# Kernel tuning notes

Hardware: AMD Instinct MI355X
Metric: run time of the kernel (lower is better)

## Reference

```python
import jax, jax.numpy as jnp
import numpy as np

LN_EPS = 1e-5
NEG_SLOPE = 0.01

def layer_norm(h, gamma, beta):
    mu = jnp.mean(h, axis=-1, keepdims=True)
    var = jnp.var(h, axis=-1, keepdims=True)
    return (h - mu) * jax.lax.rsqrt(var + LN_EPS) * gamma + beta

def setup_inputs() -> dict:
    key = jax.random.key(0)
    ks = jax.random.split(key, 12)
    N, E = 50000, 600000
    D_NODE, D_EDGE, D_IN = 128, 64, 192  # D_IN = D_NODE + D_EDGE
    x = jax.random.normal(ks[0], (N, D_NODE), dtype=jnp.float32)
    edge_index = jax.random.randint(ks[1], (2, E), 0, N, dtype=jnp.int64)
    edge_attr = jax.random.normal(ks[2], (E, D_EDGE), dtype=jnp.float32)
    # mlp_before_agg: Linear(192->128) + LayerNorm + LeakyReLU
    W1 = jax.random.normal(ks[3], (D_IN, D_NODE), dtype=jnp.float32) / np.sqrt(D_IN)
    b1 = jnp.zeros((D_NODE,), dtype=jnp.float32)
    g1 = jnp.ones((D_NODE,), dtype=jnp.float32)
    be1 = jnp.zeros((D_NODE,), dtype=jnp.float32)
    # mlp_after_agg: Linear(128->128) + LayerNorm + LeakyReLU
    W2 = jax.random.normal(ks[4], (D_NODE, D_NODE), dtype=jnp.float32) / np.sqrt(D_NODE)
    b2 = jnp.zeros((D_NODE,), dtype=jnp.float32)
    g2 = jnp.ones((D_NODE,), dtype=jnp.float32)
    be2 = jnp.zeros((D_NODE,), dtype=jnp.float32)
    return {"x": x, "edge_index": edge_index, "edge_attr": edge_attr,
            "W1": W1, "b1": b1, "g1": g1, "be1": be1,
            "W2": W2, "b2": b2, "g2": g2, "be2": be2}

def reference(x, edge_index, edge_attr, W1, b1, g1, be1, W2, b2, g2, be2):
    N = x.shape[0]
    row, col = edge_index[0], edge_index[1]
    # 1. gather + concat: (E, D_NODE + D_EDGE)
    out = jnp.concatenate([x[row], edge_attr], axis=1)
    # 2. pre-agg MLP: Linear + LayerNorm + LeakyReLU
    out = jax.nn.leaky_relu(layer_norm(out @ W1 + b1, g1, be1), NEG_SLOPE)
    # 3. scatter-mean aggregate over destination nodes (empty segments -> 0)
    sums = jax.ops.segment_sum(out, col, num_segments=N)
    counts = jax.ops.segment_sum(jnp.ones((out.shape[0], 1), out.dtype), col, num_segments=N)
    out = sums / jnp.maximum(counts, 1.0)
    # 4. post-agg MLP + residual + activation
    out = jax.nn.leaky_relu(layer_norm(out @ W2 + b2, g2, be2), NEG_SLOPE)
    return jax.nn.leaky_relu(out + x, NEG_SLOPE)
```

## Files before the change

kernel.cpp:

```cpp
#include <hip/hip_runtime.h>

#define D_NODE 128
#define D_EDGE 64
#define D_IN   192
#define NEG    0.01f
#define LN_EPS 1e-5f

typedef short bf16x8 __attribute__((ext_vector_type(8)));
typedef float f32x4  __attribute__((ext_vector_type(4)));

__device__ __forceinline__ unsigned f2bf(float f) {
    unsigned u = __builtin_bit_cast(unsigned, f);
    return (u + 0x7FFFu + ((u >> 16) & 1u)) >> 16;
}
__device__ __forceinline__ unsigned pk2(float a, float b) {
    return f2bf(a) | (f2bf(b) << 16);
}
__device__ __forceinline__ float bf2f(unsigned short s) {
    unsigned u = ((unsigned)s) << 16;
    return __builtin_bit_cast(float, u);
}

__global__ void k_hist(const int* __restrict__ ei, int* __restrict__ hist, int E) {
    int i = blockIdx.x * blockDim.x + threadIdx.x;
    int stride = gridDim.x * blockDim.x;
    for (int e = i; e < E; e += stride) atomicAdd(&hist[ei[E + e]], 1);
}

__global__ __launch_bounds__(1024) void k_scanA(const int* __restrict__ hist,
                                                int* __restrict__ base,
                                                int* __restrict__ blockTot, int N) {
    __shared__ int wsum[16], woff[16];
    const int t = threadIdx.x, b = blockIdx.x;
    const int i = b * 1024 + t;
    const int lane = t & 63, w = t >> 6;
    int v = (i < N) ? hist[i] : 0;
    int x = v;
    #pragma unroll
    for (int d = 1; d < 64; d <<= 1) { int u = __shfl_up(x, d); if (lane >= d) x += u; }
    if (lane == 63) wsum[w] = x;
    __syncthreads();
    if (t < 16) {
        int y = wsum[t];
        #pragma unroll
        for (int d = 1; d < 16; d <<= 1) { int u = __shfl_up(y, d, 16); if (t >= d) y += u; }
        woff[t] = y - wsum[t];
    }
    __syncthreads();
    int incl = x + woff[w];
    if (i < N) base[i] = incl - v;
    if (t == 1023) blockTot[b] = incl;
}

__global__ void k_scanB(int* __restrict__ blockTot, int NB) {
    int t = threadIdx.x;
    int v = (t < NB) ? blockTot[t] : 0;
    int x = v;
    #pragma unroll
    for (int d = 1; d < 64; d <<= 1) { int u = __shfl_up(x, d); if (t >= d) x += u; }
    if (t < NB) blockTot[t] = x - v;
}

__global__ __launch_bounds__(1024) void k_scanC(int* __restrict__ base,
                                                const int* __restrict__ blockTot, int N) {
    int i = blockIdx.x * 1024 + threadIdx.x;
    if (i < N) base[i] += blockTot[blockIdx.x];
}

__global__ void k_bucket(const int* __restrict__ ei, int* __restrict__ base,
                         int* __restrict__ perm, int* __restrict__ srcrow,
                         int* __restrict__ dstcol, int E) {
    int i = blockIdx.x * blockDim.x + threadIdx.x;
    int stride = gridDim.x * blockDim.x;
    for (int e = i; e < E; e += stride) {
        int c = ei[E + e];
        int r = ei[e];
        int p = atomicAdd(&base[c], 1);
        perm[p]   = e;
        srcrow[p] = r;
        dstcol[p] = c;
    }
}

__global__ __launch_bounds__(256) void edge_mfma_seg(
    const float* __restrict__ x,
    const float* __restrict__ edge_attr,
    const int*   __restrict__ perm,
    const int*   __restrict__ srcrow,
    const int*   __restrict__ dstcol,
    const float* __restrict__ W1,
    const float* __restrict__ b1,
    const float* __restrict__ g1,
    const float* __restrict__ be1,
    float* __restrict__ sums,
    int E, int ntiles)
{
    __shared__ unsigned short h[64][200];
    __shared__ float rS [64][4], rS2[64][4];
    __shared__ int   scol[64];
    __shared__ unsigned long long maskSh;

    const int tid = threadIdx.x;
    const int w   = tid >> 6;
    const int l   = tid & 63;
    const int lm  = l & 15;
    const int q   = l >> 4;
    const int q8  = q * 8;

    bf16x8 Bfr[2][6];
    float  b1v[2], g1v[2], bev[2];
    #pragma unroll
    for (int c2 = 0; c2 < 2; ++c2) {
        const int n = (2 * w + c2) * 16 + lm;
        b1v[c2] = b1[n]; g1v[c2] = g1[n]; bev[c2] = be1[n];
        #pragma unroll
        for (int kt = 0; kt < 6; ++kt) {
            bf16x8 f;
            #pragma unroll
            for (int j = 0; j < 8; ++j)
                f[j] = (short)f2bf(W1[(kt * 32 + q8 + j) * 128 + n]);
            Bfr[c2][kt] = f;
        }
    }

    for (int tile = blockIdx.x; tile < ntiles; tile += gridDim.x) {
        const int e0 = tile * 64;

        {
            const int e  = tid >> 2;
            const int qq = tid & 3;
            const int ge = e0 + e;
            if (ge < E) {
                const int row = srcrow[ge];
                const int eid = perm[ge];
                const float4* xr = (const float4*)(x + (size_t)row * D_NODE);
                #pragma unroll
                for (int i = 0; i < 8; ++i) {
                    float4 v = xr[qq * 8 + i];
                    *(uint2*)&h[e][qq * 32 + i * 4] =
                        make_uint2(pk2(v.x, v.y), pk2(v.z, v.w));
                }
                const float4* ar = (const float4*)(edge_attr + (size_t)eid * D_EDGE);
                #pragma unroll
                for (int i = 0; i < 4; ++i) {
                    float4 v = ar[qq * 4 + i];
                    *(uint2*)&h[e][128 + qq * 16 + i * 4] =
                        make_uint2(pk2(v.x, v.y), pk2(v.z, v.w));
                }
            } else {
                #pragma unroll
                for (int i = 0; i < 8; ++i)
                    *(uint2*)&h[e][qq * 32 + i * 4] = make_uint2(0u, 0u);
                #pragma unroll
                for (int i = 0; i < 4; ++i)
                    *(uint2*)&h[e][128 + qq * 16 + i * 4] = make_uint2(0u, 0u);
            }
            if (tid < 64)
                scol[tid] = (e0 + tid < E) ? dstcol[e0 + tid] : -1;
        }
        __syncthreads();

        f32x4 acc[4][2];
        #pragma unroll
        for (int et = 0; et < 4; ++et)
            #pragma unroll
            for (int c2 = 0; c2 < 2; ++c2)
                acc[et][c2] = (f32x4){0.f, 0.f, 0.f, 0.f};

        #pragma unroll
        for (int et = 0; et < 4; ++et) {
            bf16x8 Afr[6];
            #pragma unroll
            for (int kt = 0; kt < 6; ++kt)
                Afr[kt] = *(const bf16x8*)&h[et * 16 + lm][kt * 32 + q8];
            #pragma unroll
            for (int c2 = 0; c2 < 2; ++c2)
                #pragma unroll
                for (int kt = 0; kt < 6; ++kt)
                    acc[et][c2] = __builtin_amdgcn_mfma_f32_16x16x32_bf16(
                        Afr[kt], Bfr[c2][kt], acc[et][c2], 0, 0, 0);
        }

        #pragma unroll
        for (int et = 0; et < 4; ++et) {
            #pragma unroll
            for (int r = 0; r < 4; ++r) {
                float v0 = acc[et][0][r] + b1v[0];
                float v1 = acc[et][1][r] + b1v[1];
                acc[et][0][r] = v0;
                acc[et][1][r] = v1;
                float s  = v0 + v1;
                float s2 = v0 * v0 + v1 * v1;
                #pragma unroll
                for (int off = 1; off < 16; off <<= 1) {
                    s  += __shfl_xor(s,  off, 16);
                    s2 += __shfl_xor(s2, off, 16);
                }
                if (lm == 0) {
                    const int em = et * 16 + q * 4 + r;
                    rS [em][w] = s;
                    rS2[em][w] = s2;
                }
            }
        }
        __syncthreads();

        if (tid < 64) {
            int me = scol[tid];
            int pv = (tid == 0) ? (me ^ 1) : scol[tid - 1];
            unsigned long long m = __ballot(me != pv);
            if (tid == 0) maskSh = m;
        }

        #pragma unroll
        for (int et = 0; et < 4; ++et) {
            #pragma unroll
            for (int r = 0; r < 4; ++r) {
                const int em = et * 16 + q * 4 + r;
                float4 p  = *(const float4*)&rS [em][0];
                float4 p2 = *(const float4*)&rS2[em][0];
                const float S    = (p.x  + p.y)  + (p.z  + p.w);
                const float S2   = (p2.x + p2.y) + (p2.z + p2.w);
                const float mu   = S * (1.f / 128.f);
                const float var  = S2 * (1.f / 128.f) - mu * mu;
                const float rstd = rsqrtf(var + LN_EPS);
                #pragma unroll
                for (int c2 = 0; c2 < 2; ++c2) {
                    float y = (acc[et][c2][r] - mu) * rstd * g1v[c2] + bev[c2];
                    y = (y > 0.f) ? y : NEG * y;
                    h[em][(2 * w + c2) * 16 + lm] = (unsigned short)f2bf(y);
                }
            }
        }
        __syncthreads();

        {
            const unsigned long long mask = maskSh;
            const int g  = tid >> 7;
            const int j  = tid & 127;
            const int lo = g * 32, hi = lo + 32;
            float s = 0.f;
            int rs = lo;
            for (int em = lo; em < hi; ++em) {
                s += bf2f(h[em][j]);
                const int nx = em + 1;
                const bool isEnd = (nx == hi) || ((mask >> nx) & 1ull);
                if (isEnd) {
                    const int dest = scol[em];
                    if (dest >= 0) {
                        const bool sg = (rs > 0) && ((mask >> rs) & 1ull);
                        const bool eg = (em < 63) && ((mask >> nx) & 1ull);
                        float* p = &sums[(size_t)dest * D_NODE + j];
                        if (sg && eg) *p = s;
                        else          atomicAdd(p, s);
                    }
                    s = 0.f; rs = nx;
                }
            }
        }
        __syncthreads();
    }
}

__global__ __launch_bounds__(256) void node_mfma(
    const float* __restrict__ sums,
    const int*   __restrict__ hist,
    const float* __restrict__ x,
    const float* __restrict__ W2,
    const float* __restrict__ b2,
    const float* __restrict__ g2,
    const float* __restrict__ be2,
    float* __restrict__ out,
    int N)
{
    __shared__ unsigned short h[64][136];
    __shared__ float rS [64][4], rS2[64][4];

    const int tid = threadIdx.x;
    const int w   = tid >> 6;
    const int l   = tid & 63;
    const int lm  = l & 15;
    const int q   = l >> 4;
    const int q8  = q * 8;

    bf16x8 Bfr[2][4];
    float  b2v[2], g2v[2], bev[2];
    #pragma unroll
    for (int c2 = 0; c2 < 2; ++c2) {
        const int n = (2 * w + c2) * 16 + lm;
        b2v[c2] = b2[n]; g2v[c2] = g2[n]; bev[c2] = be2[n];
        #pragma unroll
        for (int kt = 0; kt < 4; ++kt) {
            bf16x8 f;
            #pragma unroll
            for (int j = 0; j < 8; ++j)
                f[j] = (short)f2bf(W2[(kt * 32 + q8 + j) * 128 + n]);
            Bfr[c2][kt] = f;
        }
    }

    const int n0 = blockIdx.x * 64;

    {
        const int e  = tid >> 2;
        const int qq = tid & 3;
        const int gn = n0 + e;
        if (gn < N) {
            const int cnt = hist[gn];
            const float sc = (cnt > 0) ? 1.f / (float)cnt : 0.f;
            const float4* sr = (const float4*)(sums + (size_t)gn * D_NODE);
            #pragma unroll
            for (int i = 0; i < 8; ++i) {
                float4 v = sr[qq * 8 + i];
                *(uint2*)&h[e][qq * 32 + i * 4] =
                    make_uint2(pk2(v.x * sc, v.y * sc), pk2(v.z * sc, v.w * sc));
            }
        } else {
            #pragma unroll
            for (int i = 0; i < 8; ++i)
                *(uint2*)&h[e][qq * 32 + i * 4] = make_uint2(0u, 0u);
        }
    }
    __syncthreads();

    f32x4 acc[4][2];
    #pragma unroll
    for (int et = 0; et < 4; ++et)
        #pragma unroll
        for (int c2 = 0; c2 < 2; ++c2)
            acc[et][c2] = (f32x4){0.f, 0.f, 0.f, 0.f};

    #pragma unroll
    for (int et = 0; et < 4; ++et) {
        bf16x8 Afr[4];
        #pragma unroll
        for (int kt = 0; kt < 4; ++kt)
            Afr[kt] = *(const bf16x8*)&h[et * 16 + lm][kt * 32 + q8];
        #pragma unroll
        for (int c2 = 0; c2 < 2; ++c2)
            #pragma unroll
            for (int kt = 0; kt < 4; ++kt)
                acc[et][c2] = __builtin_amdgcn_mfma_f32_16x16x32_bf16(
                    Afr[kt], Bfr[c2][kt], acc[et][c2], 0, 0, 0);
    }

    #pragma unroll
    for (int et = 0; et < 4; ++et) {
        #pragma unroll
        for (int r = 0; r < 4; ++r) {
            float v0 = acc[et][0][r] + b2v[0];
            float v1 = acc[et][1][r] + b2v[1];
            acc[et][0][r] = v0;
            acc[et][1][r] = v1;
            float s  = v0 + v1;
            float s2 = v0 * v0 + v1 * v1;
            #pragma unroll
            for (int off = 1; off < 16; off <<= 1) {
                s  += __shfl_xor(s,  off, 16);
                s2 += __shfl_xor(s2, off, 16);
            }
            if (lm == 0) {
                const int em = et * 16 + q * 4 + r;
                rS [em][w] = s;
                rS2[em][w] = s2;
            }
        }
    }
    __syncthreads();

    #pragma unroll
    for (int et = 0; et < 4; ++et) {
        #pragma unroll
        for (int r = 0; r < 4; ++r) {
            const int em = et * 16 + q * 4 + r;
            const int gn = n0 + em;
            if (gn >= N) continue;
            float4 p  = *(const float4*)&rS [em][0];
            float4 p2 = *(const float4*)&rS2[em][0];
            const float S    = (p.x  + p.y)  + (p.z  + p.w);
            const float S2   = (p2.x + p2.y) + (p2.z + p2.w);
            const float mu   = S * (1.f / 128.f);
            const float var  = S2 * (1.f / 128.f) - mu * mu;
            const float rstd = rsqrtf(var + LN_EPS);
            #pragma unroll
            for (int c2 = 0; c2 < 2; ++c2) {
                const int col = (2 * w + c2) * 16 + lm;
                float y = (acc[et][c2][r] - mu) * rstd * g2v[c2] + bev[c2];
                y = (y > 0.f) ? y : NEG * y;
                float rr = y + x[(size_t)gn * D_NODE + col];
                rr = (rr > 0.f) ? rr : NEG * rr;
                out[(size_t)gn * D_NODE + col] = rr;
            }
        }
    }
}

extern "C" void kernel_launch(void* const* d_in, const int* in_sizes, int n_in,
                              void* d_out, int out_size, void* d_ws, size_t ws_size,
                              hipStream_t stream) {
    const float* x          = (const float*)d_in[0];
    const int*   edge_index = (const int*)  d_in[1];
    const float* edge_attr  = (const float*)d_in[2];
    const float* W1         = (const float*)d_in[3];
    const float* b1         = (const float*)d_in[4];
    const float* g1         = (const float*)d_in[5];
    const float* be1        = (const float*)d_in[6];
    const float* W2         = (const float*)d_in[7];
    const float* b2         = (const float*)d_in[8];
    const float* g2         = (const float*)d_in[9];
    const float* be2        = (const float*)d_in[10];

    const int N = in_sizes[0] / D_NODE;
    const int E = in_sizes[1] / 2;

    float* sums     = (float*)d_ws;
    int*   hist     = (int*)(sums + (size_t)N * D_NODE);
    int*   base     = hist + N;
    int*   blockTot = base + N;
    int*   perm     = blockTot + 64;
    int*   srcrow   = perm + E;
    int*   dstcol   = srcrow + E;

    hipMemsetAsync(d_ws, 0, ((size_t)N * D_NODE + (size_t)N) * sizeof(float), stream);

    k_hist<<<dim3(256), dim3(256), 0, stream>>>(edge_index, hist, E);
    const int NB = (N + 1023) / 1024;
    k_scanA<<<dim3(NB), dim3(1024), 0, stream>>>(hist, base, blockTot, N);
    k_scanB<<<dim3(1),  dim3(64),   0, stream>>>(blockTot, NB);
    k_scanC<<<dim3(NB), dim3(1024), 0, stream>>>(base, blockTot, N);
    k_bucket<<<dim3(256), dim3(256), 0, stream>>>(edge_index, base, perm, srcrow, dstcol, E);

    const int ntiles = (E + 63) / 64;
    const int grid   = ntiles < 1280 ? ntiles : 1280;
    edge_mfma_seg<<<dim3(grid), dim3(256), 0, stream>>>(
        x, edge_attr, perm, srcrow, dstcol, W1, b1, g1, be1, sums, E, ntiles);

    node_mfma<<<dim3((N + 63) / 64), dim3(256), 0, stream>>>(
        sums, hist, x, W2, b2, g2, be2, (float*)d_out, N);
}
```

Measured before the change: 509.7 us.

## Replace prefix scan with atomic bucket allocation and pack edge records

The three-kernel prefix scan is replaced by one kernel where each node claims its bucket range with an atomicAdd on a global cursor. Buckets are therefore no longer ordered by node index, but each remains contiguous. The perm, srcrow and dstcol arrays are packed into one 8-byte record per edge, with src and dst squeezed into 16 bits each. This cuts launches and the number of separate index loads, but the 16-bit packing only works while N stays below 65536. Grid sizes for hist and bucket are also doubled.

Measured after the change: 520.0 us. 1.02x slower.

```diff
diff --git a/kernel.cpp b/kernel.cpp
--- a/kernel.cpp
+++ b/kernel.cpp
@@ -27,67 +27,28 @@
     for (int e = i; e < E; e += stride) atomicAdd(&hist[ei[E + e]], 1);
 }
 
-__global__ __launch_bounds__(1024) void k_scanA(const int* __restrict__ hist,
-                                                int* __restrict__ base,
-                                                int* __restrict__ blockTot, int N) {
-    __shared__ int wsum[16], woff[16];
-    const int t = threadIdx.x, b = blockIdx.x;
-    const int i = b * 1024 + t;
-    const int lane = t & 63, w = t >> 6;
-    int v = (i < N) ? hist[i] : 0;
-    int x = v;
-    #pragma unroll
-    for (int d = 1; d < 64; d <<= 1) { int u = __shfl_up(x, d); if (lane >= d) x += u; }
-    if (lane == 63) wsum[w] = x;
-    __syncthreads();
-    if (t < 16) {
-        int y = wsum[t];
-        #pragma unroll
-        for (int d = 1; d < 16; d <<= 1) { int u = __shfl_up(y, d, 16); if (t >= d) y += u; }
-        woff[t] = y - wsum[t];
-    }
-    __syncthreads();
-    int incl = x + woff[w];
-    if (i < N) base[i] = incl - v;
-    if (t == 1023) blockTot[b] = incl;
-}
-
-__global__ void k_scanB(int* __restrict__ blockTot, int NB) {
-    int t = threadIdx.x;
-    int v = (t < NB) ? blockTot[t] : 0;
-    int x = v;
-    #pragma unroll
-    for (int d = 1; d < 64; d <<= 1) { int u = __shfl_up(x, d); if (t >= d) x += u; }
-    if (t < NB) blockTot[t] = x - v;
-}
-
-__global__ __launch_bounds__(1024) void k_scanC(int* __restrict__ base,
-                                                const int* __restrict__ blockTot, int N) {
-    int i = blockIdx.x * 1024 + threadIdx.x;
-    if (i < N) base[i] += blockTot[blockIdx.x];
+__global__ void k_alloc(const int* __restrict__ hist, int* __restrict__ base,
+                        int* __restrict__ cursor, int N) {
+    int i = blockIdx.x * blockDim.x + threadIdx.x;
+    if (i < N) base[i] = atomicAdd(cursor, hist[i]);
 }
 
 __global__ void k_bucket(const int* __restrict__ ei, int* __restrict__ base,
-                         int* __restrict__ perm, int* __restrict__ srcrow,
-                         int* __restrict__ dstcol, int E) {
+                         uint2* __restrict__ recs, int E) {
     int i = blockIdx.x * blockDim.x + threadIdx.x;
     int stride = gridDim.x * blockDim.x;
     for (int e = i; e < E; e += stride) {
         int c = ei[E + e];
         int r = ei[e];
         int p = atomicAdd(&base[c], 1);
-        perm[p]   = e;
-        srcrow[p] = r;
-        dstcol[p] = c;
+        recs[p] = make_uint2((unsigned)e, (unsigned)r | ((unsigned)c << 16));
     }
 }
 
 __global__ __launch_bounds__(256) void edge_mfma_seg(
     const float* __restrict__ x,
     const float* __restrict__ edge_attr,
-    const int*   __restrict__ perm,
-    const int*   __restrict__ srcrow,
-    const int*   __restrict__ dstcol,
+    const uint2* __restrict__ recs,
     const float* __restrict__ W1,
     const float* __restrict__ b1,
     const float* __restrict__ g1,
@@ -131,8 +92,9 @@
             const int qq = tid & 3;
             const int ge = e0 + e;
             if (ge < E) {
-                const int row = srcrow[ge];
-                const int eid = perm[ge];
+                const uint2 rc = recs[ge];
+                const int eid = (int)rc.x;
+                const int row = (int)(rc.y & 0xFFFFu);
                 const float4* xr = (const float4*)(x + (size_t)row * D_NODE);
                 #pragma unroll
                 for (int i = 0; i < 8; ++i) {
@@ -156,7 +118,7 @@
                     *(uint2*)&h[e][128 + qq * 16 + i * 4] = make_uint2(0u, 0u);
             }
             if (tid < 64)
-                scol[tid] = (e0 + tid < E) ? dstcol[e0 + tid] : -1;
+                scol[tid] = (e0 + tid < E) ? (int)(recs[e0 + tid].y >> 16) : -1;
         }
         __syncthreads();
 
@@ -413,27 +375,22 @@
     const int N = in_sizes[0] / D_NODE;
     const int E = in_sizes[1] / 2;
 
-    float* sums     = (float*)d_ws;
-    int*   hist     = (int*)(sums + (size_t)N * D_NODE);
-    int*   base     = hist + N;
-    int*   blockTot = base + N;
-    int*   perm     = blockTot + 64;
-    int*   srcrow   = perm + E;
-    int*   dstcol   = srcrow + E;
-
-    hipMemsetAsync(d_ws, 0, ((size_t)N * D_NODE + (size_t)N) * sizeof(float), stream);
-
-    k_hist<<<dim3(256), dim3(256), 0, stream>>>(edge_index, hist, E);
-    const int NB = (N + 1023) / 1024;
-    k_scanA<<<dim3(NB), dim3(1024), 0, stream>>>(hist, base, blockTot, N);
-    k_scanB<<<dim3(1),  dim3(64),   0, stream>>>(blockTot, NB);
-    k_scanC<<<dim3(NB), dim3(1024), 0, stream>>>(base, blockTot, N);
-    k_bucket<<<dim3(256), dim3(256), 0, stream>>>(edge_index, base, perm, srcrow, dstcol, E);
+    uint2* recs   = (uint2*)d_ws;
+    float* sums   = (float*)(recs + E);
+    int*   hist   = (int*)(sums + (size_t)N * D_NODE);
+    int*   cursor = hist + N;
+    int*   base   = cursor + 1;
+
+    hipMemsetAsync(sums, 0, ((size_t)N * D_NODE + N + 1) * sizeof(float), stream);
+
+    k_hist  <<<dim3(512), dim3(256), 0, stream>>>(edge_index, hist, E);
+    k_alloc <<<dim3((N + 255) / 256), dim3(256), 0, stream>>>(hist, base, cursor, N);
+    k_bucket<<<dim3(512), dim3(256), 0, stream>>>(edge_index, base, recs, E);
 
     const int ntiles = (E + 63) / 64;
     const int grid   = ntiles < 1280 ? ntiles : 1280;
     edge_mfma_seg<<<dim3(grid), dim3(256), 0, stream>>>(
-        x, edge_attr, perm, srcrow, dstcol, W1, b1, g1, be1, sums, E, ntiles);
+        x, edge_attr, recs, W1, b1, g1, be1, sums, E, ntiles);
 
     node_mfma<<<dim3((N + 63) / 64), dim3(256), 0, stream>>>(
         sums, hist, x, W2, b2, g2, be2, (float*)d_out, N);
```
